# Performance work log

Measured on AMD Instinct MI355X. Metric: run time of the kernel, lower is better.

The kernel has to match this reference:

```python
import jax, jax.numpy as jnp
import numpy as np

N_IN, N_OUT, K, G = 128, 128, 3, 8
BATCH = 512
GRID_MIN, GRID_MAX = -1.0, 1.0
EDGES = N_IN * N_OUT


def setup_inputs() -> dict:
    key = jax.random.key(0)
    k1, k2 = jax.random.split(key)
    # inputs inside the grid range so splines are active
    x = jax.random.uniform(k1, (BATCH, N_IN), dtype=jnp.float32,
                           minval=GRID_MIN, maxval=GRID_MAX)
    # per-edge extended uniform knot vector: G+2K+1 points (k extra on each side)
    h = (GRID_MAX - GRID_MIN) / G
    knots_1d = jnp.linspace(GRID_MIN - K * h, GRID_MAX + K * h,
                            G + 2 * K + 1, dtype=jnp.float32)
    knots = jnp.broadcast_to(knots_1d, (EDGES, G + 2 * K + 1))
    c_basis = (jax.random.normal(k2, (EDGES, G + K), dtype=jnp.float32) * 0.1)
    c_spl = jnp.ones((N_OUT, N_IN), jnp.float32)
    c_res = jnp.ones((N_OUT, N_IN), jnp.float32)
    bias = jnp.zeros((N_OUT,), jnp.float32)
    return {"x": x, "knots": knots, "c_basis": c_basis,
            "c_spl": c_spl, "c_res": c_res, "bias": bias}


def _extend(x):
    # (batch, n_in) -> (edges, batch) with edge index = o*n_in + i
    batch = x.shape[0]
    return jnp.broadcast_to(x[:, None, :], (batch, N_OUT, N_IN)).reshape(batch, EDGES).T


def _basis(x, knots):
    # Cox-de Boor recursion; returns (edges, G+K, batch)
    x_ext = _extend(x)                   # (edges, batch)
    grid = knots[:, :, None]             # (edges, G+2K+1, 1)
    x_in = x_ext[:, None, :]             # (edges, 1, batch)
    b = ((x_in >= grid[:, :-1]) & (x_in < grid[:, 1:])).astype(jnp.float32)
    for order in range(1, K + 1):
        left = (x_in - grid[:, :-(order + 1)]) / (grid[:, order:-1] - grid[:, :-(order + 1)])
        right = (grid[:, order + 1:] - x_in) / (grid[:, order + 1:] - grid[:, 1:-order])
        b = left * b[:, :-1] + right * b[:, 1:]
    return b


def reference(x, knots, c_basis, c_spl, c_res, bias):
    batch = x.shape[0]
    bi = _basis(x, knots)                           # (edges, G+K, batch)
    spl = jnp.einsum('eg,egb->eb', c_basis, bi).T   # (batch, edges)
    y = c_spl.reshape(1, EDGES) * spl
    x_ext = _extend(x).T                            # (batch, edges)
    y = y + c_res.reshape(1, EDGES) * jax.nn.silu(x_ext)
    y = jnp.sum(y.reshape(batch, N_OUT, N_IN), axis=2) + bias
    return y
```

## Files before the change

kernel.cpp:

```cpp
#include <hip/hip_runtime.h>
#include <math.h>

#define N_IN  128
#define N_OUT 128
#define BATCH 512
#define NK    11
#define TB    8
#define TO    8

__global__ __launch_bounds__(256) void kan_kernel(
    const float* __restrict__ x,
    const float* __restrict__ cbasis,
    const float* __restrict__ cspl,
    const float* __restrict__ cres,
    const float* __restrict__ bias,
    float* __restrict__ y)
{
    __shared__ float sBv[TB * 516];
    __shared__ float sEx[TB * 258];
    __shared__ float sCW[TO * 258];
    __shared__ float sRed[256];

    const int b0 = blockIdx.x * TB;
    const int o0 = blockIdx.y * TO;
    const int t  = threadIdx.x;

    for (int p = t; p < TB * N_IN; p += 256) {
        const int b_l = p >> 7, i = p & 127;
        const float xv = x[(b0 + b_l) * N_IN + i];
        const float u  = (xv + 1.75f) * 4.0f;
        float jf = floorf(u);
        jf = fminf(fmaxf(jf, 3.0f), 10.0f);
        const float tt  = u - jf;
        const float omt = 1.0f - tt;
        const float t2 = tt * tt, t3 = t2 * tt;
        const float B0 = omt * omt * omt * (1.0f / 6.0f);
        const float B1 = (3.0f * t3 - 6.0f * t2 + 4.0f) * (1.0f / 6.0f);
        const float B2 = (-3.0f * t3 + 3.0f * t2 + 3.0f * tt + 1.0f) * (1.0f / 6.0f);
        const float B3 = t3 * (1.0f / 6.0f);
        const int base = (int)jf - 3;
        const float sig  = 1.0f / (1.0f + __expf(-xv));
        const float silu = xv * sig;
        *(float4*)&sBv[b_l * 516 + i * 4] = make_float4(B0, B1, B2, B3);
        *(float2*)&sEx[b_l * 258 + i * 2] = make_float2(silu, __int_as_float(base));
    }
    for (int p = t; p < TO * N_IN; p += 256) {
        const int o_l = p >> 7, i = p & 127;
        const int g = (o0 + o_l) * N_IN + i;
        *(float2*)&sCW[o_l * 258 + i * 2] = make_float2(cspl[g], cres[g]);
    }
    __syncthreads();

    const int b_l = t & 7;
    const int o_l = (t >> 3) & 7;
    const int h   = t >> 6;
    const int o   = o0 + o_l;
    const int i0  = h * 32;

    const float2* exBase = (const float2*)&sEx[b_l * 258];
    const float4* bvBase = (const float4*)&sBv[b_l * 516];
    const float2* cwBase = (const float2*)&sCW[o_l * 258];
    const float*  cb     = cbasis + (size_t)(o * N_IN + i0) * NK;

    float acc = 0.0f;
#pragma unroll 8
    for (int ii = 0; ii < 32; ++ii) {
        const int i = i0 + ii;
        const float2 ex = exBase[i];
        const float4 bv = bvBase[i];
        const float2 cw = cwBase[i];
        const int base  = __float_as_int(ex.y);
        float4 cv;
        __builtin_memcpy(&cv, cb + base, 16);
        const float spl = cv.x * bv.x + cv.y * bv.y + cv.z * bv.z + cv.w * bv.w;
        acc = fmaf(cw.x, spl, acc);
        acc = fmaf(cw.y, ex.x, acc);
        cb += NK;
    }

    sRed[t] = acc;
    __syncthreads();
    if (h == 0) {
        const float tot = sRed[t] + sRed[t + 64] + sRed[t + 128] + sRed[t + 192]
                        + bias[o];
        y[(b0 + b_l) * N_OUT + o] = tot;
    }
}

extern "C" void kernel_launch(void* const* d_in, const int* in_sizes, int n_in,
                              void* d_out, int out_size, void* d_ws, size_t ws_size,
                              hipStream_t stream) {
    const float* x      = (const float*)d_in[0];
    const float* cbasis = (const float*)d_in[2];
    const float* cspl   = (const float*)d_in[3];
    const float* cres   = (const float*)d_in[4];
    const float* bias   = (const float*)d_in[5];
    float* y = (float*)d_out;

    dim3 grid(BATCH / TB, N_OUT / TO);
    kan_kernel<<<grid, 256, 0, stream>>>(x, cbasis, cspl, cres, bias, y);
}
```

Baseline: 71.19 us.

## Prebuild aligned per-window coefficient table with c_spl folded in

Adds a pre-pass kernel that builds, for each edge, 8 aligned float4 windows of basis coefficients already scaled by c_spl, stored in the workspace. The main kernel then does one aligned 16-byte load per edge instead of an unaligned 4-float load from the stride-11 array, and drops the c_spl shared-memory staging. The cost is an extra launch each call and about 2MB of extra memory traffic for the expanded table, which is rebuilt every call.

```diff
diff --git a/kernel.cpp b/kernel.cpp
--- a/kernel.cpp
+++ b/kernel.cpp
@@ -8,17 +8,29 @@
 #define TB    8
 #define TO    8
 
+__global__ __launch_bounds__(256) void w4_build(
+    const float* __restrict__ cbasis,
+    const float* __restrict__ cspl,
+    float* __restrict__ w4)
+{
+    const int t = blockIdx.x * 256 + threadIdx.x;
+    const int e = t >> 3, slot = t & 7;
+    const float s = cspl[e];
+    const float* r = cbasis + e * NK + slot;
+    float4 v = make_float4(s * r[0], s * r[1], s * r[2], s * r[3]);
+    *(float4*)(w4 + (size_t)t * 4) = v;
+}
+
 __global__ __launch_bounds__(256) void kan_kernel(
     const float* __restrict__ x,
-    const float* __restrict__ cbasis,
-    const float* __restrict__ cspl,
+    const float* __restrict__ w4,
     const float* __restrict__ cres,
     const float* __restrict__ bias,
     float* __restrict__ y)
 {
     __shared__ float sBv[TB * 516];
     __shared__ float sEx[TB * 258];
-    __shared__ float sCW[TO * 258];
+    __shared__ float sCW[TO * 129];
     __shared__ float sRed[256];
 
     const int b0 = blockIdx.x * TB;
@@ -38,16 +50,15 @@
         const float B1 = (3.0f * t3 - 6.0f * t2 + 4.0f) * (1.0f / 6.0f);
         const float B2 = (-3.0f * t3 + 3.0f * t2 + 3.0f * tt + 1.0f) * (1.0f / 6.0f);
         const float B3 = t3 * (1.0f / 6.0f);
-        const int base = (int)jf - 3;
+        const int boff = ((int)jf - 3) * 4;
         const float sig  = 1.0f / (1.0f + __expf(-xv));
         const float silu = xv * sig;
         *(float4*)&sBv[b_l * 516 + i * 4] = make_float4(B0, B1, B2, B3);
-        *(float2*)&sEx[b_l * 258 + i * 2] = make_float2(silu, __int_as_float(base));
+        *(float2*)&sEx[b_l * 258 + i * 2] = make_float2(silu, __int_as_float(boff));
     }
     for (int p = t; p < TO * N_IN; p += 256) {
         const int o_l = p >> 7, i = p & 127;
-        const int g = (o0 + o_l) * N_IN + i;
-        *(float2*)&sCW[o_l * 258 + i * 2] = make_float2(cspl[g], cres[g]);
+        sCW[o_l * 129 + i] = cres[(o0 + o_l) * N_IN + i];
     }
     __syncthreads();
 
@@ -59,8 +70,8 @@
 
     const float2* exBase = (const float2*)&sEx[b_l * 258];
     const float4* bvBase = (const float4*)&sBv[b_l * 516];
-    const float2* cwBase = (const float2*)&sCW[o_l * 258];
-    const float*  cb     = cbasis + (size_t)(o * N_IN + i0) * NK;
+    const float*  cwBase = &sCW[o_l * 129];
+    const float*  w4row  = w4 + ((size_t)(o * N_IN + i0) << 5);
 
     float acc = 0.0f;
 #pragma unroll 8
@@ -68,14 +79,15 @@
         const int i = i0 + ii;
         const float2 ex = exBase[i];
         const float4 bv = bvBase[i];
-        const float2 cw = cwBase[i];
-        const int base  = __float_as_int(ex.y);
-        float4 cv;
-        __builtin_memcpy(&cv, cb + base, 16);
-        const float spl = cv.x * bv.x + cv.y * bv.y + cv.z * bv.z + cv.w * bv.w;
-        acc = fmaf(cw.x, spl, acc);
-        acc = fmaf(cw.y, ex.x, acc);
-        cb += NK;
+        const float cr  = cwBase[i];
+        const int boff  = __float_as_int(ex.y);
+        const float4 cv = *(const float4*)(w4row + boff);
+        acc = fmaf(cv.x, bv.x, acc);
+        acc = fmaf(cv.y, bv.y, acc);
+        acc = fmaf(cv.z, bv.z, acc);
+        acc = fmaf(cv.w, bv.w, acc);
+        acc = fmaf(cr, ex.x, acc);
+        w4row += 32;
     }
 
     sRed[t] = acc;
@@ -95,8 +107,10 @@
     const float* cspl   = (const float*)d_in[3];
     const float* cres   = (const float*)d_in[4];
     const float* bias   = (const float*)d_in[5];
-    float* y = (float*)d_out;
+    float* y  = (float*)d_out;
+    float* w4 = (float*)d_ws;
 
+    w4_build<<<512, 256, 0, stream>>>(cbasis, cspl, w4);
     dim3 grid(BATCH / TB, N_OUT / TO);
-    kan_kernel<<<grid, 256, 0, stream>>>(x, cbasis, cspl, cres, bias, y);
+    kan_kernel<<<grid, 256, 0, stream>>>(x, w4, cres, bias, y);
 }
```

Result: slower. 74.59 us (+4.8%).

## Stage c_basis pre-scaled by c_spl in LDS and recompute B-spline weights inline

Applied to the files above, without the earlier changes.

Each block now copies its 8 output rows of c_basis into shared memory, multiplied by c_spl, so the inner loop reads coefficients from LDS instead of issuing unaligned per-thread global loads. Per-input data is packed as one float2 holding silu and base+0.5*t, and the four cubic basis weights are recomputed in the inner loop instead of being stored as float4 in shared memory. This removes redundant global traffic and folds the c_spl multiply into staging, at the cost of about 45KB of LDS per block (lower occupancy), a serial global-to-LDS staging phase, and extra ALU work per inner iteration.

```diff
diff --git a/kernel.cpp b/kernel.cpp
--- a/kernel.cpp
+++ b/kernel.cpp
@@ -7,6 +7,7 @@
 #define NK    11
 #define TB    8
 #define TO    8
+#define CBS   1412
 
 __global__ __launch_bounds__(256) void kan_kernel(
     const float* __restrict__ x,
@@ -16,38 +17,37 @@
     const float* __restrict__ bias,
     float* __restrict__ y)
 {
-    __shared__ float sBv[TB * 516];
-    __shared__ float sEx[TB * 258];
-    __shared__ float sCW[TO * 258];
-    __shared__ float sRed[256];
+    __shared__ float  sCB[TO * CBS];
+    __shared__ float2 sEx[TB * 130];
+    __shared__ float  sCR[TO * 129];
+    __shared__ float  sRed[256];
 
     const int b0 = blockIdx.x * TB;
     const int o0 = blockIdx.y * TO;
     const int t  = threadIdx.x;
 
+    for (int o_l = 0; o_l < TO; ++o_l) {
+        const int erow = (o0 + o_l) * N_IN;
+        const float* src = cbasis + (size_t)erow * NK;
+        for (int p = t; p < N_IN * NK; p += 256) {
+            const int i = (unsigned)p / NK;
+            sCB[o_l * CBS + p] = src[p] * cspl[erow + i];
+        }
+    }
     for (int p = t; p < TB * N_IN; p += 256) {
         const int b_l = p >> 7, i = p & 127;
         const float xv = x[(b0 + b_l) * N_IN + i];
         const float u  = (xv + 1.75f) * 4.0f;
         float jf = floorf(u);
         jf = fminf(fmaxf(jf, 3.0f), 10.0f);
-        const float tt  = u - jf;
-        const float omt = 1.0f - tt;
-        const float t2 = tt * tt, t3 = t2 * tt;
-        const float B0 = omt * omt * omt * (1.0f / 6.0f);
-        const float B1 = (3.0f * t3 - 6.0f * t2 + 4.0f) * (1.0f / 6.0f);
-        const float B2 = (-3.0f * t3 + 3.0f * t2 + 3.0f * tt + 1.0f) * (1.0f / 6.0f);
-        const float B3 = t3 * (1.0f / 6.0f);
+        const float tt = u - jf;
         const int base = (int)jf - 3;
         const float sig  = 1.0f / (1.0f + __expf(-xv));
-        const float silu = xv * sig;
-        *(float4*)&sBv[b_l * 516 + i * 4] = make_float4(B0, B1, B2, B3);
-        *(float2*)&sEx[b_l * 258 + i * 2] = make_float2(silu, __int_as_float(base));
+        sEx[b_l * 130 + i] = make_float2(xv * sig, (float)base + 0.5f * tt);
     }
     for (int p = t; p < TO * N_IN; p += 256) {
         const int o_l = p >> 7, i = p & 127;
-        const int g = (o0 + o_l) * N_IN + i;
-        *(float2*)&sCW[o_l * 258 + i * 2] = make_float2(cspl[g], cres[g]);
+        sCR[o_l * 129 + i] = cres[(o0 + o_l) * N_IN + i];
     }
     __syncthreads();
 
@@ -57,25 +57,33 @@
     const int o   = o0 + o_l;
     const int i0  = h * 32;
 
-    const float2* exBase = (const float2*)&sEx[b_l * 258];
-    const float4* bvBase = (const float4*)&sBv[b_l * 516];
-    const float2* cwBase = (const float2*)&sCW[o_l * 258];
-    const float*  cb     = cbasis + (size_t)(o * N_IN + i0) * NK;
+    const float2* exBase = &sEx[b_l * 130];
+    const float*  crBase = &sCR[o_l * 129];
+    const float*  cbBase = &sCB[o_l * CBS];
 
     float acc = 0.0f;
-#pragma unroll 8
+#pragma unroll 4
     for (int ii = 0; ii < 32; ++ii) {
         const int i = i0 + ii;
         const float2 ex = exBase[i];
-        const float4 bv = bvBase[i];
-        const float2 cw = cwBase[i];
-        const int base  = __float_as_int(ex.y);
-        float4 cv;
-        __builtin_memcpy(&cv, cb + base, 16);
-        const float spl = cv.x * bv.x + cv.y * bv.y + cv.z * bv.z + cv.w * bv.w;
-        acc = fmaf(cw.x, spl, acc);
-        acc = fmaf(cw.y, ex.x, acc);
-        cb += NK;
+        const float cr  = crBase[i];
+        const float fb = truncf(ex.y);
+        const int base = (int)fb;
+        const float tt = (ex.y - fb) * 2.0f;
+        const float t2  = tt * tt;
+        const float t3  = t2 * tt;
+        const float omt = 1.0f - tt;
+        const float B0  = omt * omt * omt * (1.0f / 6.0f);
+        const float B1  = fmaf(0.5f, t3, (2.0f / 3.0f)) - t2;
+        const float B3  = t3 * (1.0f / 6.0f);
+        const float B2  = 1.0f - B0 - B1 - B3;
+        const float* c = cbBase + i * NK + base;
+        float spl = c[0] * B0;
+        spl = fmaf(c[1], B1, spl);
+        spl = fmaf(c[2], B2, spl);
+        spl = fmaf(c[3], B3, spl);
+        acc += spl;
+        acc = fmaf(cr, ex.x, acc);
     }
 
     sRed[t] = acc;
```

Result: slower. 100.1 us (+40.7%).

## Recast KAN layer as sparse-expanded bf16 MFMA GEMM over basis and silu features

Applied to the files above, without the earlier changes.

Each input is expanded into a 12-wide feature vector: the four cubic B-spline weights are scattered into their slots of an 11-slot basis row, and silu(x) goes in the last slot. The kernel converts these features and the matching weights (c_spl times c_basis, plus c_res) to bf16 in LDS and computes the output with 16x16x32 bf16 MFMA instructions over 16x16 output tiles. This replaces the scalar gather-FMA loop with matrix-core work, at the cost of redundant multiplies on zero basis slots and bf16 rounding of both operands. The basis and weight conversion is redone per block, and the feature tile is zero-filled in LDS for each half of the input dimension.

```diff
diff --git a/kernel.cpp b/kernel.cpp
--- a/kernel.cpp
+++ b/kernel.cpp
@@ -5,8 +5,18 @@
 #define N_OUT 128
 #define BATCH 512
 #define NK    11
-#define TB    8
-#define TO    8
+#define TBV   16
+#define TOV   16
+#define STR   776
+
+typedef float f32x4  __attribute__((ext_vector_type(4)));
+typedef short bf16x8 __attribute__((ext_vector_type(8)));
+
+__device__ __forceinline__ unsigned short f2bf(float f) {
+    unsigned u = __float_as_uint(f);
+    u += 0x7FFFu + ((u >> 16) & 1u);
+    return (unsigned short)(u >> 16);
+}
 
 __global__ __launch_bounds__(256) void kan_kernel(
     const float* __restrict__ x,
@@ -16,74 +26,89 @@
     const float* __restrict__ bias,
     float* __restrict__ y)
 {
-    __shared__ float sBv[TB * 516];
-    __shared__ float sEx[TB * 258];
-    __shared__ float sCW[TO * 258];
-    __shared__ float sRed[256];
+    __shared__ short sA[TBV * STR];
+    __shared__ short sW[TOV * STR];
+    __shared__ float sAcc[4 * 256];
 
-    const int b0 = blockIdx.x * TB;
-    const int o0 = blockIdx.y * TO;
+    const int b0 = blockIdx.x * TBV;
+    const int o0 = blockIdx.y * TOV;
     const int t  = threadIdx.x;
+    const int w  = t >> 6;
+    const int l  = t & 63;
+    const int mn = l & 15;
+    const int kq = (l >> 4) * 8;
 
-    for (int p = t; p < TB * N_IN; p += 256) {
-        const int b_l = p >> 7, i = p & 127;
-        const float xv = x[(b0 + b_l) * N_IN + i];
-        const float u  = (xv + 1.75f) * 4.0f;
-        float jf = floorf(u);
-        jf = fminf(fmaxf(jf, 3.0f), 10.0f);
-        const float tt  = u - jf;
-        const float omt = 1.0f - tt;
-        const float t2 = tt * tt, t3 = t2 * tt;
-        const float B0 = omt * omt * omt * (1.0f / 6.0f);
-        const float B1 = (3.0f * t3 - 6.0f * t2 + 4.0f) * (1.0f / 6.0f);
-        const float B2 = (-3.0f * t3 + 3.0f * t2 + 3.0f * tt + 1.0f) * (1.0f / 6.0f);
-        const float B3 = t3 * (1.0f / 6.0f);
-        const int base = (int)jf - 3;
-        const float sig  = 1.0f / (1.0f + __expf(-xv));
-        const float silu = xv * sig;
-        *(float4*)&sBv[b_l * 516 + i * 4] = make_float4(B0, B1, B2, B3);
-        *(float2*)&sEx[b_l * 258 + i * 2] = make_float2(silu, __int_as_float(base));
-    }
-    for (int p = t; p < TO * N_IN; p += 256) {
-        const int o_l = p >> 7, i = p & 127;
-        const int g = (o0 + o_l) * N_IN + i;
-        *(float2*)&sCW[o_l * 258 + i * 2] = make_float2(cspl[g], cres[g]);
-    }
-    __syncthreads();
+    f32x4 acc = {0.f, 0.f, 0.f, 0.f};
 
-    const int b_l = t & 7;
-    const int o_l = (t >> 3) & 7;
-    const int h   = t >> 6;
-    const int o   = o0 + o_l;
-    const int i0  = h * 32;
+    for (int hh = 0; hh < 2; ++hh) {
+        for (int p = t; p < (TBV * STR) / 8; p += 256)
+            *(int4*)&sA[p * 8] = make_int4(0, 0, 0, 0);
+        __syncthreads();
 
-    const float2* exBase = (const float2*)&sEx[b_l * 258];
-    const float4* bvBase = (const float4*)&sBv[b_l * 516];
-    const float2* cwBase = (const float2*)&sCW[o_l * 258];
-    const float*  cb     = cbasis + (size_t)(o * N_IN + i0) * NK;
+        for (int p = t; p < TBV * 64; p += 256) {
+            const int b  = p >> 6, il = p & 63;
+            const int i  = hh * 64 + il;
+            const float xv = x[(b0 + b) * N_IN + i];
+            const float u  = (xv + 1.75f) * 4.0f;
+            float jf = floorf(u);
+            jf = fminf(fmaxf(jf, 3.0f), 10.0f);
+            const float tt = u - jf;
+            const float omt = 1.0f - tt;
+            const float t2 = tt * tt, t3 = t2 * tt;
+            const float B0 = omt * omt * omt * (1.0f / 6.0f);
+            const float B1 = (3.0f * t3 - 6.0f * t2 + 4.0f) * (1.0f / 6.0f);
+            const float B2 = (-3.0f * t3 + 3.0f * t2 + 3.0f * tt + 1.0f) * (1.0f / 6.0f);
+            const float B3 = t3 * (1.0f / 6.0f);
+            const int base = (int)jf - 3;
+            const float sig = 1.0f / (1.0f + __expf(-xv));
+            short* dst = &sA[b * STR + il * 12];
+            dst[base]     = (short)f2bf(B0);
+            dst[base + 1] = (short)f2bf(B1);
+            dst[base + 2] = (short)f2bf(B2);
+            dst[base + 3] = (short)f2bf(B3);
+            dst[11]       = (short)f2bf(xv * sig);
+        }
 
-    float acc = 0.0f;
-#pragma unroll 8
-    for (int ii = 0; ii < 32; ++ii) {
-        const int i = i0 + ii;
-        const float2 ex = exBase[i];
-        const float4 bv = bvBase[i];
-        const float2 cw = cwBase[i];
-        const int base  = __float_as_int(ex.y);
-        float4 cv;
-        __builtin_memcpy(&cv, cb + base, 16);
-        const float spl = cv.x * bv.x + cv.y * bv.y + cv.z * bv.z + cv.w * bv.w;
-        acc = fmaf(cw.x, spl, acc);
-        acc = fmaf(cw.y, ex.x, acc);
-        cb += NK;
+        for (int p = t; p < TOV * 64; p += 256) {
+            const int o_l = p >> 6, il = p & 63;
+            const int i   = hh * 64 + il;
+            const int e   = (o0 + o_l) * N_IN + i;
+            const float s = cspl[e];
+            const float* src = cbasis + (size_t)e * NK;
+            unsigned short hv[12];
+            #pragma unroll
+            for (int g = 0; g < 11; ++g) hv[g] = f2bf(s * src[g]);
+            hv[11] = f2bf(cres[e]);
+            unsigned d[6];
+            #pragma unroll
+            for (int j = 0; j < 6; ++j)
+                d[j] = (unsigned)hv[2 * j] | ((unsigned)hv[2 * j + 1] << 16);
+            short* dst = &sW[o_l * STR + il * 12];
+            *(uint2*)(dst)     = make_uint2(d[0], d[1]);
+            *(uint2*)(dst + 4) = make_uint2(d[2], d[3]);
+            *(uint2*)(dst + 8) = make_uint2(d[4], d[5]);
+        }
+        __syncthreads();
+
+        const short* aB = &sA[mn * STR + w * 192 + kq];
+        const short* bB = &sW[mn * STR + w * 192 + kq];
+        #pragma unroll
+        for (int s = 0; s < 6; ++s) {
+            bf16x8 af  = *(const bf16x8*)(aB + s * 32);
+            bf16x8 bf_ = *(const bf16x8*)(bB + s * 32);
+            acc = __builtin_amdgcn_mfma_f32_16x16x32_bf16(af, bf_, acc, 0, 0, 0);
+        }
+        __syncthreads();
     }
 
-    sRed[t] = acc;
+    #pragma unroll
+    for (int r = 0; r < 4; ++r)
+        sAcc[w * 256 + ((l >> 4) * 4 + r) * 16 + mn] = acc[r];
     __syncthreads();
-    if (h == 0) {
-        const float tot = sRed[t] + sRed[t + 64] + sRed[t + 128] + sRed[t + 192]
-                        + bias[o];
-        y[(b0 + b_l) * N_OUT + o] = tot;
+    {
+        const int m2 = t >> 4, n2 = t & 15;
+        const float sum = sAcc[t] + sAcc[256 + t] + sAcc[512 + t] + sAcc[768 + t];
+        y[(b0 + m2) * N_OUT + (o0 + n2)] = sum + bias[o0 + n2];
     }
 }
 
@@ -97,6 +122,6 @@
     const float* bias   = (const float*)d_in[5];
     float* y = (float*)d_out;
 
-    dim3 grid(BATCH / TB, N_OUT / TO);
+    dim3 grid(BATCH / TBV, N_OUT / TOV);
     kan_kernel<<<grid, 256, 0, stream>>>(x, cbasis, cspl, cres, bias, y);
 }
```

Result: no change. 71.35 us (+0.2%).
